# Performance work log

Hardware: AMD Instinct MI355X
Metric: run time of the kernel (lower is better)

The kernel has to match this reference:

```python
import jax, jax.numpy as jnp
import numpy as np

T = 2048          # num tokens
H_DIM = 2048      # hidden_size
NUM_HEADS = 32    # linear_num_value_heads
NUM_KV = 16       # linear_num_key_heads
DK = 128          # linear_key_head_dim
DV = 128          # linear_value_head_dim
KCONV = 4         # linear_conv_kernel_dim
KEY_DIM = NUM_KV * DK       # 2048
VAL_DIM = NUM_HEADS * DV    # 4096
CHUNK = 64


def setup_inputs() -> dict:
    key = jax.random.key(0)
    ks = jax.random.split(key, 14)
    s = 0.02
    return {
        "hidden_states": jax.random.normal(ks[0], (T, H_DIM), jnp.float32),
        "Wq": jax.random.normal(ks[1], (H_DIM, KEY_DIM), jnp.float32) * s,
        "Wk": jax.random.normal(ks[2], (H_DIM, KEY_DIM), jnp.float32) * s,
        "Wv": jax.random.normal(ks[3], (H_DIM, VAL_DIM), jnp.float32) * s,
        "Wa": jax.random.normal(ks[4], (H_DIM, NUM_HEADS), jnp.float32) * s,
        "Wb": jax.random.normal(ks[5], (H_DIM, NUM_HEADS), jnp.float32) * s,
        "Wg": jax.random.normal(ks[6], (H_DIM, VAL_DIM), jnp.float32) * s,
        "conv_q": jax.random.normal(ks[7], (KEY_DIM, KCONV), jnp.float32) * 0.3,
        "conv_k": jax.random.normal(ks[8], (KEY_DIM, KCONV), jnp.float32) * 0.3,
        "conv_v": jax.random.normal(ks[9], (VAL_DIM, KCONV), jnp.float32) * 0.3,
        "dt_bias": jax.random.normal(ks[10], (NUM_HEADS,), jnp.float32) * 0.1,
        "A_log": jnp.log(jax.random.uniform(ks[11], (NUM_HEADS,), jnp.float32, 1.0, 8.0)),
        "o_norm_weight": 1.0 + 0.1 * jax.random.normal(ks[12], (DV,), jnp.float32),
        "Wo": jax.random.normal(ks[13], (VAL_DIM, H_DIM), jnp.float32) * s,
    }


def _causal_depthwise_conv(x, w):
    # x: [T, C], w: [C, K] -> causal depthwise conv, output [T, C]
    K = w.shape[1]
    xp = jnp.pad(x, ((K - 1, 0), (0, 0)))
    out = jax.lax.conv_general_dilated(
        xp.T[None], w[:, None, :], window_strides=(1,), padding='VALID',
        dimension_numbers=('NCH', 'OIH', 'NCH'), feature_group_count=w.shape[0])
    return out[0].T


def _l2norm(x, eps=1e-6):
    return x * jax.lax.rsqrt(jnp.sum(x * x, axis=-1, keepdims=True) + eps)


def _gdn_core(q, k, v, g, beta):
    # q,k: [T,H,DK]; v: [T,H,DV]; g,beta: [T,H]. Gated delta-rule recurrence,
    # scanned in chunks (rematerialized inner scan = chunked selective scan).
    def step(S, inp):
        qt, kt, vt, gt, bt = inp
        S = S * jnp.exp(gt)[:, None, None]                  # decay state [H,DK,DV]
        kv = jnp.einsum('hk,hkv->hv', kt, S)                # read memory at k
        dv = bt[:, None] * (vt - kv)                        # delta update
        S = S + kt[:, :, None] * dv[:, None, :]             # write outer(k, dv)
        o = jnp.einsum('hk,hkv->hv', qt, S)                 # read at q
        return S, o

    def chunk_fn(S, ch):
        return jax.lax.scan(step, S, ch)

    def resh(x):
        return x.reshape(T // CHUNK, CHUNK, *x.shape[1:])

    xs = (resh(q), resh(k), resh(v), resh(g), resh(beta))
    S0 = jnp.zeros((NUM_HEADS, DK, DV), jnp.float32)
    _, o = jax.lax.scan(jax.checkpoint(chunk_fn), S0, xs)
    return o.reshape(T, NUM_HEADS, DV)


def reference(hidden_states, Wq, Wk, Wv, Wa, Wb, Wg, conv_q, conv_k, conv_v,
              dt_bias, A_log, o_norm_weight, Wo):
    h = hidden_states
    # projections
    mixed = jnp.concatenate([h @ Wq, h @ Wk, h @ Wv], axis=-1)
    # fused causal depthwise conv1d + silu over concatenated qkv
    wconv = jnp.concatenate([conv_q, conv_k, conv_v], axis=0)
    mixed = _causal_depthwise_conv(mixed, wconv)
    mixed = mixed * jax.nn.sigmoid(mixed)  # silu activation
    q, k, v = jnp.split(mixed, [KEY_DIM, 2 * KEY_DIM], axis=-1)
    q = q.reshape(T, NUM_KV, DK)
    k = k.reshape(T, NUM_KV, DK)
    v = v.reshape(T, NUM_HEADS, DV)
    ratio = NUM_HEADS // NUM_KV
    q = jnp.repeat(q, ratio, axis=1)   # GQA expand (repeat-interleave)
    k = jnp.repeat(k, ratio, axis=1)
    q = _l2norm(q)
    k = _l2norm(k)
    # fused gating: g = -exp(A_log) * softplus(a + dt_bias); beta = sigmoid(b)
    x = h @ Wa + dt_bias
    sp = jnp.where(x <= 20.0, jax.nn.softplus(x), x)  # threshold=20, beta=1
    g = -jnp.exp(A_log) * sp                          # [T, H]
    beta = jax.nn.sigmoid(h @ Wb)                     # allow_neg_eigval=False
    o = _gdn_core(q * (DK ** -0.5), k, v, g, beta)
    # gated RMSNorm (norm before gate), eps=1e-5
    gate = (h @ Wg).reshape(T, NUM_HEADS, DV)
    o = o * jax.lax.rsqrt(jnp.mean(o * o, axis=-1, keepdims=True) + 1e-5) * o_norm_weight
    o = o * (gate * jax.nn.sigmoid(gate))
    return o.reshape(T, VAL_DIM) @ Wo
```

## Files before the change

### kernel.cpp

```cpp
#include <hip/hip_runtime.h>
#include <hip/hip_bf16.h>
#include <stdint.h>
#include <stddef.h>

using bf16 = __hip_bfloat16;
typedef __attribute__((ext_vector_type(8))) short short8;
typedef __attribute__((ext_vector_type(4))) float f32x4;
typedef __attribute__((ext_vector_type(2))) float f32x2;

#define T_TOK 2048
#define HD    2048
#define NH    32
#define NKV   16
#define DKh   128
#define DVh   128

__device__ __forceinline__ void bf2f(uint32_t u, float& a, float& b) {
    union { uint32_t i; float f; } x;
    x.i = u << 16;          a = x.f;
    x.i = u & 0xffff0000u;  b = x.f;
}

__device__ __forceinline__ void gload16(const void* g, void* l) {
    __builtin_amdgcn_global_load_lds(
        (const __attribute__((address_space(1))) void*)g,
        (__attribute__((address_space(3))) void*)l, 16, 0, 0);
}

__device__ __forceinline__ void store_c(bf16* C, size_t off, float v) { C[off] = __float2bfloat16(v); }
__device__ __forceinline__ void store_c(float* C, size_t off, float v) { C[off] = v; }

template <int CTRL>
__device__ __forceinline__ float dppadd(float x) {
    int y = __builtin_amdgcn_update_dpp(0, __float_as_int(x), CTRL, 0xf, 0xf, true);
    return x + __int_as_float(y);
}
__device__ __forceinline__ void red16x2(float& x, float& y) {
    x = dppadd<0xB1>(x);  y = dppadd<0xB1>(y);
    x = dppadd<0x4E>(x);  y = dppadd<0x4E>(y);
    x = dppadd<0x141>(x); y = dppadd<0x141>(y);
    x = dppadd<0x140>(x); y = dppadd<0x140>(y);
}

__device__ __forceinline__ f32x2 pkfma(f32x2 a, f32x2 b, f32x2 c) {
    return __builtin_elementwise_fma(a, b, c);
}

__global__ __launch_bounds__(256) void f2b_kernel(
    const float* __restrict__ in, bf16* __restrict__ out, int n)
{
    int i = blockIdx.x * 256 + threadIdx.x;
    if (i < n) out[i] = __float2bfloat16(in[i]);
}

__global__ __launch_bounds__(256) void transpose_kernel(
    const float* __restrict__ in, bf16* __restrict__ out, int R, int C)
{
    __shared__ bf16 tile[32][33];
    int c0 = blockIdx.x * 32, r0 = blockIdx.y * 32;
    int x = threadIdx.x;
    int y = threadIdx.y;
    #pragma unroll
    for (int i = y; i < 32; i += 8)
        tile[i][x] = __float2bfloat16(in[(size_t)(r0 + i) * C + c0 + x]);
    __syncthreads();
    #pragma unroll
    for (int i = y; i < 32; i += 8)
        out[(size_t)(c0 + i) * R + r0 + x] = tile[x][i];
}

__global__ __launch_bounds__(256) void build_wab_kernel(
    const float* __restrict__ Wa, const float* __restrict__ Wb, bf16* __restrict__ out)
{
    int k = blockIdx.x * 256 + threadIdx.x;
    int n = blockIdx.y;
    float v = 0.f;
    if (n < 32)      v = Wa[(size_t)k * 32 + n];
    else if (n < 64) v = Wb[(size_t)k * 32 + (n - 32)];
    out[(size_t)n * 2048 + k] = __float2bfloat16(v);
}

template <typename OutT>
__global__ __launch_bounds__(256) void gemm_bt_kernel(
    const bf16* __restrict__ A, const bf16* __restrict__ B, OutT* __restrict__ C,
    int M, int N, int K)
{
    __shared__ short sA[128 * 64];
    __shared__ short sB[128 * 64];
    const int tid  = threadIdx.x;
    const int w    = tid >> 6;
    const int lane = tid & 63;
    const int quad = lane >> 4;
    const int r    = lane & 15;
    const int wm   = w >> 1, wn = w & 1;
    const int bm   = blockIdx.x, bn = blockIdx.y;
    const int lrow = lane >> 3;
    const int lp   = lane & 7;
    const int lc   = lp ^ lrow;

    f32x4 acc[4][4] = {};

    const int nkb = K >> 6;
    for (int kb = 0; kb < nkb; ++kb) {
        __syncthreads();
        #pragma unroll
        for (int it = 0; it < 4; ++it) {
            int grp = w * 4 + it;
            int rr  = grp * 8 + lrow;
            const bf16* ga = A + (size_t)(bm * 128 + rr) * K + kb * 64 + lc * 8;
            gload16(ga, (void*)(sA + grp * 512));
            const bf16* gb = B + (size_t)(bn * 128 + rr) * K + kb * 64 + lc * 8;
            gload16(gb, (void*)(sB + grp * 512));
        }
        __syncthreads();

        #pragma unroll
        for (int kk = 0; kk < 2; ++kk) {
            short8 av[4], bv[4];
            #pragma unroll
            for (int i = 0; i < 4; ++i) {
                int p   = (kk * 4 + quad) ^ (r & 7);
                int row = wm * 64 + i * 16 + r;
                av[i] = *(const short8*)(sA + row * 64 + p * 8);
                int rowb = wn * 64 + i * 16 + r;
                bv[i] = *(const short8*)(sB + rowb * 64 + p * 8);
            }
            #pragma unroll
            for (int i = 0; i < 4; ++i)
                #pragma unroll
                for (int j = 0; j < 4; ++j)
                    acc[i][j] = __builtin_amdgcn_mfma_f32_16x16x32_bf16(
                        av[i], bv[j], acc[i][j], 0, 0, 0);
        }
    }

    #pragma unroll
    for (int i = 0; i < 4; ++i) {
        int row0 = bm * 128 + wm * 64 + i * 16 + quad * 4;
        #pragma unroll
        for (int j = 0; j < 4; ++j) {
            int col = bn * 128 + wn * 64 + j * 16 + r;
            #pragma unroll
            for (int e = 0; e < 4; ++e)
                store_c(C, (size_t)(row0 + e) * N + col, acc[i][j][e]);
        }
    }
}

__global__ __launch_bounds__(128) void conv_qk_kernel(
    const bf16* __restrict__ mixed, const float* __restrict__ cq,
    const float* __restrict__ ck, float* __restrict__ qn, float* __restrict__ kn,
    float* __restrict__ pk4)
{
    int t   = blockIdx.x;
    int hkv = blockIdx.y;
    int d   = threadIdx.x;
    int cl  = hkv * DKh + d;
    float aq = 0.f, ak = 0.f;
    #pragma unroll
    for (int j = 0; j < 4; ++j) {
        int ts = t - 3 + j;
        if (ts >= 0) {
            aq += __bfloat162float(mixed[(size_t)ts * 8192 + cl])        * cq[cl * 4 + j];
            ak += __bfloat162float(mixed[(size_t)ts * 8192 + 2048 + cl]) * ck[cl * 4 + j];
        }
    }
    float sq = aq / (1.f + __expf(-aq));
    float sk = ak / (1.f + __expf(-ak));
    float s0 = sq * sq, s1 = sk * sk, s2 = sq * sk;
    #pragma unroll
    for (int m = 1; m < 64; m <<= 1) {
        s0 += __shfl_xor(s0, m, 64);
        s1 += __shfl_xor(s1, m, 64);
        s2 += __shfl_xor(s2, m, 64);
    }
    __shared__ float part[6];
    if ((threadIdx.x & 63) == 0) {
        int w = threadIdx.x >> 6;
        part[w * 3 + 0] = s0; part[w * 3 + 1] = s1; part[w * 3 + 2] = s2;
    }
    __syncthreads();
    float sumq = part[0] + part[3];
    float sumk = part[1] + part[4];
    float sqk  = part[2] + part[5];
    float rnq = rsqrtf(sumq + 1e-6f);
    float rnk = rsqrtf(sumk + 1e-6f);
    const float scale = 0.08838834764831845f;
    qn[(size_t)t * 2048 + cl] = sq * rnq * scale;
    kn[(size_t)t * 2048 + cl] = sk * rnk;
    if (d == 0) {
        float qk = sqk * rnq * rnk * scale;
        pk4[((size_t)(2 * hkv)     * T_TOK + t) * 4 + 3] = qk;
        pk4[((size_t)(2 * hkv + 1) * T_TOK + t) * 4 + 3] = qk;
    }
}

__global__ __launch_bounds__(256) void conv_v_kernel(
    const bf16* __restrict__ mixed, const float* __restrict__ cv, bf16* __restrict__ vv)
{
    int idx = blockIdx.x * 256 + threadIdx.x;
    int t = idx >> 12, c = idx & 4095;
    float acc = 0.f;
    #pragma unroll
    for (int j = 0; j < 4; ++j) {
        int ts = t - 3 + j;
        if (ts >= 0)
            acc += __bfloat162float(mixed[(size_t)ts * 8192 + 4096 + c]) * cv[c * 4 + j];
    }
    vv[idx] = __float2bfloat16(acc / (1.f + __expf(-acc)));
}

__global__ __launch_bounds__(256) void gating_kernel(
    const float* __restrict__ ab, const float* __restrict__ dt_bias,
    const float* __restrict__ A_log, float* __restrict__ pk4)
{
    int i = blockIdx.x * 256 + threadIdx.x;
    int h = i >> 11, t = i & 2047;
    float a  = ab[(size_t)t * 128 + h] + dt_bias[h];
    float sp = (a <= 20.f) ? log1pf(__expf(a)) : a;
    float gg = -__expf(A_log[h]) * sp;
    float b  = ab[(size_t)t * 128 + 32 + h];
    float eg = __expf(gg);
    float be = 1.f / (1.f + __expf(-b));
    size_t base = ((size_t)h * T_TOK + t) * 4;
    pk4[base + 0] = eg;
    pk4[base + 1] = -be * eg;
    pk4[base + 2] = be;
}

__device__ __forceinline__ void gdn_step(
    f32x2 S[4], float4 kfa, float4 kfb, float4 qfa, float4 qfb,
    float egt, float nbt, float bvt, float qkt, bf16* optr, bool writer)
{
    f32x2 k2[4] = {{kfa.x, kfa.y}, {kfa.z, kfa.w}, {kfb.x, kfb.y}, {kfb.z, kfb.w}};
    f32x2 q2[4] = {{qfa.x, qfa.y}, {qfa.z, qfa.w}, {qfb.x, qfb.y}, {qfb.z, qfb.w}};
    f32x2 pd = pkfma(S[1], k2[1], S[0] * k2[0]);
    f32x2 pe = pkfma(S[3], k2[3], S[2] * k2[2]);
    f32x2 qd = pkfma(S[1], q2[1], S[0] * q2[0]);
    f32x2 qe = pkfma(S[3], q2[3], S[2] * q2[2]);
    f32x2 e2 = {egt, egt};
    f32x2 Se0 = S[0] * e2, Se1 = S[1] * e2, Se2 = S[2] * e2, Se3 = S[3] * e2;
    f32x2 ps = pd + pe;
    f32x2 qs = qd + qe;
    float d1 = ps.x + ps.y;
    float d2 = qs.x + qs.y;
    red16x2(d1, d2);
    float dvv = fmaf(nbt, d1, bvt);
    f32x2 dv2 = {dvv, dvv};
    S[0] = pkfma(k2[0], dv2, Se0);
    S[1] = pkfma(k2[1], dv2, Se1);
    S[2] = pkfma(k2[2], dv2, Se2);
    S[3] = pkfma(k2[3], dv2, Se3);
    if (writer) *optr = __float2bfloat16(fmaf(qkt, dvv, egt * d2));
}

#define TILE 16

__global__ __launch_bounds__(256, 1) void recur_kernel(
    const float* __restrict__ qn, const float* __restrict__ kn, const bf16* __restrict__ vv,
    const float* __restrict__ pk4, bf16* __restrict__ o)
{
    __shared__ float    skq[2][TILE][256];
    __shared__ float    sgt[2][TILE][4];
    __shared__ uint16_t sv2[2][TILE][16];

    int h    = blockIdx.x;
    int sp   = blockIdx.y;
    int tid  = threadIdx.x;
    int dvl  = tid >> 4;
    int dkg  = tid & 15;
    int dv   = sp * 16 + dvl;
    int hkv  = h >> 1;
    int wave = tid >> 6;
    int lane = tid & 63;
    bool writer = (dkg == 0);

    bf16* optr = o + (size_t)h * DVh + dv;

    const float* kqsrc = (lane < 32)
        ? (kn + (size_t)hkv * DKh + (size_t)lane * 4)
        : (qn + (size_t)hkv * DKh + (size_t)(lane - 32) * 4);
    const bf16*  vsrc  = vv + (size_t)h * DVh + sp * 16 + (size_t)(lane & 1) * 8;
    const float* gsrc  = pk4 + ((size_t)h * T_TOK) * 4;

    f32x2 S[4] = {};

    auto stage = [&](int b, int t0) {
        #pragma unroll
        for (int i = 0; i < 4; ++i) {
            int tok = wave * 4 + i;
            gload16(kqsrc + (size_t)(t0 + tok) * 2048, (void*)&skq[b][tok][0]);
        }
        if (wave == 0) {
            if (lane < 32)
                gload16(vsrc + (size_t)(t0 + (lane >> 1)) * 4096, (void*)&sv2[b][0][0]);
        } else if (wave == 1) {
            if (lane < 16)
                gload16(gsrc + (size_t)(t0 + lane) * 4, (void*)&sgt[b][0][0]);
        }
    };

    stage(0, 0);
    __syncthreads();

    int buf = 0;
    #pragma unroll 1
    for (int t0 = 0; t0 < T_TOK; t0 += TILE) {
        stage(buf ^ 1, t0 + TILE);
        #pragma unroll
        for (int s = 0; s < TILE; ++s) {
            const float* tokp = &skq[buf][s][0];
            float4 kA = *(const float4*)(tokp + dkg * 4);
            float4 kB = *(const float4*)(tokp + 64 + dkg * 4);
            float4 qA = *(const float4*)(tokp + 128 + dkg * 4);
            float4 qB = *(const float4*)(tokp + 192 + dkg * 4);
            float4 g4 = *(const float4*)(&sgt[buf][s][0]);
            uint32_t vu = sv2[buf][s][dvl];
            float vf = __uint_as_float(vu << 16);
            float bvt = g4.z * vf;
            gdn_step(S, kA, kB, qA, qB, g4.x, g4.y, bvt, g4.w,
                     optr + (size_t)(t0 + s) * 4096, writer);
        }
        __syncthreads();
        buf ^= 1;
    }
}

__global__ __launch_bounds__(256) void normgate_kernel(
    const bf16* __restrict__ o, const bf16* __restrict__ gate,
    const float* __restrict__ w, bf16* __restrict__ og)
{
    int grp  = blockIdx.x * 4 + (threadIdx.x >> 6);
    int lane = threadIdx.x & 63;
    int t = grp >> 5, h = grp & 31;
    size_t base = (size_t)t * 4096 + h * DVh;
    uint32_t uo = *(const uint32_t*)(o + base + lane * 2);
    float a, b; bf2f(uo, a, b);
    float ss = a * a + b * b;
    #pragma unroll
    for (int m = 1; m < 64; m <<= 1) ss += __shfl_xor(ss, m, 64);
    float rn = rsqrtf(ss * (1.f / 128.f) + 1e-5f);
    uint32_t ug = *(const uint32_t*)(gate + base + lane * 2);
    float ga, gb; bf2f(ug, ga, gb);
    float wa = w[lane * 2], wb = w[lane * 2 + 1];
    float oa = a * rn * wa * (ga / (1.f + __expf(-ga)));
    float ob = b * rn * wb * (gb / (1.f + __expf(-gb)));
    og[base + lane * 2]     = __float2bfloat16(oa);
    og[base + lane * 2 + 1] = __float2bfloat16(ob);
}

extern "C" void kernel_launch(void* const* d_in, const int* in_sizes, int n_in,
                              void* d_out, int out_size, void* d_ws, size_t ws_size,
                              hipStream_t stream)
{
    const float* h       = (const float*)d_in[0];
    const float* Wq      = (const float*)d_in[1];
    const float* Wk      = (const float*)d_in[2];
    const float* Wv      = (const float*)d_in[3];
    const float* Wa      = (const float*)d_in[4];
    const float* Wb      = (const float*)d_in[5];
    const float* Wg      = (const float*)d_in[6];
    const float* conv_q  = (const float*)d_in[7];
    const float* conv_k  = (const float*)d_in[8];
    const float* conv_v  = (const float*)d_in[9];
    const float* dt_bias = (const float*)d_in[10];
    const float* A_log   = (const float*)d_in[11];
    const float* onw     = (const float*)d_in[12];
    const float* Wo      = (const float*)d_in[13];
    float* out = (float*)d_out;

    char* ws = (char*)d_ws;
    bf16*  WqkvT = (bf16*)ws;   ws += (size_t)8192 * 2048 * 2;
    bf16*  WgT   = (bf16*)ws;   ws += (size_t)4096 * 2048 * 2;
    bf16*  WoT   = (bf16*)ws;   ws += (size_t)2048 * 4096 * 2;
    bf16*  WabT  = (bf16*)ws;   ws += (size_t)128 * 2048 * 2;
    bf16*  hb    = (bf16*)ws;   ws += (size_t)2048 * 2048 * 2;
    bf16*  mixed = (bf16*)ws;   ws += (size_t)2048 * 8192 * 2;
    float* ab    = (float*)ws;  ws += (size_t)2048 * 128 * 4;
    float* knb   = (float*)ws;  ws += (size_t)2048 * 2048 * 4;
    bf16*  vvb   = (bf16*)ws;   ws += (size_t)2048 * 4096 * 2;
    float* pk4   = (float*)ws;  ws += (size_t)NH * T_TOK * 4 * 4;
    ws += 32768;
    float* qnb = (float*)WgT;
    bf16*  ob   = WqkvT;
    bf16*  gate = WqkvT + (size_t)2048 * 4096;
    bf16*  og   = mixed;

    dim3 tb(32, 8);
    transpose_kernel<<<dim3(64, 64),  tb, 0, stream>>>(Wq, WqkvT,                       2048, 2048);
    transpose_kernel<<<dim3(64, 64),  tb, 0, stream>>>(Wk, WqkvT + (size_t)2048 * 2048, 2048, 2048);
    transpose_kernel<<<dim3(128, 64), tb, 0, stream>>>(Wv, WqkvT + (size_t)4096 * 2048, 2048, 4096);
    transpose_kernel<<<dim3(128, 64), tb, 0, stream>>>(Wg, WgT,                         2048, 4096);
    transpose_kernel<<<dim3(64, 128), tb, 0, stream>>>(Wo, WoT,                         4096, 2048);
    build_wab_kernel<<<dim3(8, 128), 256, 0, stream>>>(Wa, Wb, WabT);
    f2b_kernel<<<16384, 256, 0, stream>>>(h, hb, 2048 * 2048);

    gemm_bt_kernel<bf16> <<<dim3(16, 64), 256, 0, stream>>>(hb, WqkvT, mixed, 2048, 8192, 2048);
    gemm_bt_kernel<float><<<dim3(16, 1),  256, 0, stream>>>(hb, WabT,  ab,    2048, 128,  2048);
    gemm_bt_kernel<bf16> <<<dim3(16, 32), 256, 0, stream>>>(hb, WgT,   gate,  2048, 4096, 2048);

    conv_qk_kernel<<<dim3(2048, 16), 128, 0, stream>>>(mixed, conv_q, conv_k, qnb, knb, pk4);
    conv_v_kernel<<<32768, 256, 0, stream>>>(mixed, conv_v, vvb);
    gating_kernel<<<256, 256, 0, stream>>>(ab, dt_bias, A_log, pk4);

    recur_kernel<<<dim3(32, 8), 256, 0, stream>>>(qnb, knb, vvb, pk4, ob);
    normgate_kernel<<<16384, 256, 0, stream>>>(ob, gate, onw, og);

    gemm_bt_kernel<float><<<dim3(16, 16), 256, 0, stream>>>(og, WoT, out, 2048, 2048, 4096);
}
```

Baseline: 951.6 us.

## Process recurrence two tokens per step using precomputed cross-token dot products

Rewrites the gated delta-rule recurrence to advance two tokens at once. Both tokens' S·k and S·q reductions are issued against the same state and combined into one DPP reduction. A new kernel precomputes k_t·k_{t-1} and q_t·k_{t-1} so the second token's terms can be corrected algebraically, and the state update for the pair is fused. This roughly halves the serial reduction-latency chain per token, at the cost of an extra kernel launch, extra staged data, and a different floating-point summation order.

```diff
diff --git a/kernel.cpp b/kernel.cpp
--- a/kernel.cpp
+++ b/kernel.cpp
@@ -35,16 +35,17 @@
     int y = __builtin_amdgcn_update_dpp(0, __float_as_int(x), CTRL, 0xf, 0xf, true);
     return x + __int_as_float(y);
 }
-__device__ __forceinline__ void red16x2(float& x, float& y) {
-    x = dppadd<0xB1>(x);  y = dppadd<0xB1>(y);
-    x = dppadd<0x4E>(x);  y = dppadd<0x4E>(y);
-    x = dppadd<0x141>(x); y = dppadd<0x141>(y);
-    x = dppadd<0x140>(x); y = dppadd<0x140>(y);
+__device__ __forceinline__ void red16x4(float& a, float& b, float& c, float& d) {
+    a = dppadd<0xB1>(a);  b = dppadd<0xB1>(b);  c = dppadd<0xB1>(c);  d = dppadd<0xB1>(d);
+    a = dppadd<0x4E>(a);  b = dppadd<0x4E>(b);  c = dppadd<0x4E>(c);  d = dppadd<0x4E>(d);
+    a = dppadd<0x141>(a); b = dppadd<0x141>(b); c = dppadd<0x141>(c); d = dppadd<0x141>(d);
+    a = dppadd<0x140>(a); b = dppadd<0x140>(b); c = dppadd<0x140>(c); d = dppadd<0x140>(d);
 }
 
 __device__ __forceinline__ f32x2 pkfma(f32x2 a, f32x2 b, f32x2 c) {
     return __builtin_elementwise_fma(a, b, c);
 }
+__device__ __forceinline__ f32x2 sp2(float x) { return f32x2{x, x}; }
 
 __global__ __launch_bounds__(256) void f2b_kernel(
     const float* __restrict__ in, bf16* __restrict__ out, int n)
@@ -195,6 +196,37 @@
     }
 }
 
+__global__ __launch_bounds__(128) void xterm_kernel(
+    const float* __restrict__ qn, const float* __restrict__ kn, float* __restrict__ pcx)
+{
+    int t   = blockIdx.x * 2 + 1;
+    int hkv = blockIdx.y;
+    int cl  = hkv * DKh + threadIdx.x;
+    float kc = kn[(size_t)t * 2048 + cl];
+    float kp = kn[(size_t)(t - 1) * 2048 + cl];
+    float qc = qn[(size_t)t * 2048 + cl];
+    float s1 = kc * kp, s2 = qc * kp;
+    #pragma unroll
+    for (int m = 1; m < 64; m <<= 1) {
+        s1 += __shfl_xor(s1, m, 64);
+        s2 += __shfl_xor(s2, m, 64);
+    }
+    __shared__ float part[4];
+    if ((threadIdx.x & 63) == 0) {
+        int w = threadIdx.x >> 6;
+        part[w * 2 + 0] = s1; part[w * 2 + 1] = s2;
+    }
+    __syncthreads();
+    if (threadIdx.x == 0) {
+        float kk = part[0] + part[2];
+        float qp = part[1] + part[3];
+        size_t b0 = ((size_t)(2 * hkv)     * T_TOK + t) * 2;
+        size_t b1 = ((size_t)(2 * hkv + 1) * T_TOK + t) * 2;
+        pcx[b0] = kk; pcx[b0 + 1] = qp;
+        pcx[b1] = kk; pcx[b1 + 1] = qp;
+    }
+}
+
 __global__ __launch_bounds__(256) void conv_v_kernel(
     const bf16* __restrict__ mixed, const float* __restrict__ cv, bf16* __restrict__ vv)
 {
@@ -228,40 +260,15 @@
     pk4[base + 2] = be;
 }
 
-__device__ __forceinline__ void gdn_step(
-    f32x2 S[4], float4 kfa, float4 kfb, float4 qfa, float4 qfb,
-    float egt, float nbt, float bvt, float qkt, bf16* optr, bool writer)
-{
-    f32x2 k2[4] = {{kfa.x, kfa.y}, {kfa.z, kfa.w}, {kfb.x, kfb.y}, {kfb.z, kfb.w}};
-    f32x2 q2[4] = {{qfa.x, qfa.y}, {qfa.z, qfa.w}, {qfb.x, qfb.y}, {qfb.z, qfb.w}};
-    f32x2 pd = pkfma(S[1], k2[1], S[0] * k2[0]);
-    f32x2 pe = pkfma(S[3], k2[3], S[2] * k2[2]);
-    f32x2 qd = pkfma(S[1], q2[1], S[0] * q2[0]);
-    f32x2 qe = pkfma(S[3], q2[3], S[2] * q2[2]);
-    f32x2 e2 = {egt, egt};
-    f32x2 Se0 = S[0] * e2, Se1 = S[1] * e2, Se2 = S[2] * e2, Se3 = S[3] * e2;
-    f32x2 ps = pd + pe;
-    f32x2 qs = qd + qe;
-    float d1 = ps.x + ps.y;
-    float d2 = qs.x + qs.y;
-    red16x2(d1, d2);
-    float dvv = fmaf(nbt, d1, bvt);
-    f32x2 dv2 = {dvv, dvv};
-    S[0] = pkfma(k2[0], dv2, Se0);
-    S[1] = pkfma(k2[1], dv2, Se1);
-    S[2] = pkfma(k2[2], dv2, Se2);
-    S[3] = pkfma(k2[3], dv2, Se3);
-    if (writer) *optr = __float2bfloat16(fmaf(qkt, dvv, egt * d2));
-}
-
 #define TILE 16
 
 __global__ __launch_bounds__(256, 1) void recur_kernel(
     const float* __restrict__ qn, const float* __restrict__ kn, const bf16* __restrict__ vv,
-    const float* __restrict__ pk4, bf16* __restrict__ o)
+    const float* __restrict__ pk4, const float* __restrict__ pcx, bf16* __restrict__ o)
 {
     __shared__ float    skq[2][TILE][256];
     __shared__ float    sgt[2][TILE][4];
+    __shared__ float    sgx[2][TILE][2];
     __shared__ uint16_t sv2[2][TILE][16];
 
     int h    = blockIdx.x;
@@ -282,6 +289,7 @@
         : (qn + (size_t)hkv * DKh + (size_t)(lane - 32) * 4);
     const bf16*  vsrc  = vv + (size_t)h * DVh + sp * 16 + (size_t)(lane & 1) * 8;
     const float* gsrc  = pk4 + ((size_t)h * T_TOK) * 4;
+    const float* xsrc  = pcx + ((size_t)h * T_TOK) * 2;
 
     f32x2 S[4] = {};
 
@@ -297,6 +305,9 @@
         } else if (wave == 1) {
             if (lane < 16)
                 gload16(gsrc + (size_t)(t0 + lane) * 4, (void*)&sgt[b][0][0]);
+        } else if (wave == 2) {
+            if (lane < 8)
+                gload16(xsrc + (size_t)(t0 + lane * 2) * 2, (void*)&sgx[b][0][0]);
         }
     };
 
@@ -308,18 +319,69 @@
     for (int t0 = 0; t0 < T_TOK; t0 += TILE) {
         stage(buf ^ 1, t0 + TILE);
         #pragma unroll
-        for (int s = 0; s < TILE; ++s) {
-            const float* tokp = &skq[buf][s][0];
-            float4 kA = *(const float4*)(tokp + dkg * 4);
-            float4 kB = *(const float4*)(tokp + 64 + dkg * 4);
-            float4 qA = *(const float4*)(tokp + 128 + dkg * 4);
-            float4 qB = *(const float4*)(tokp + 192 + dkg * 4);
-            float4 g4 = *(const float4*)(&sgt[buf][s][0]);
-            uint32_t vu = sv2[buf][s][dvl];
-            float vf = __uint_as_float(vu << 16);
-            float bvt = g4.z * vf;
-            gdn_step(S, kA, kB, qA, qB, g4.x, g4.y, bvt, g4.w,
-                     optr + (size_t)(t0 + s) * 4096, writer);
+        for (int p = 0; p < TILE / 2; ++p) {
+            int s0 = 2 * p, s1 = s0 + 1;
+            const float* tp0 = &skq[buf][s0][0];
+            const float* tp1 = &skq[buf][s1][0];
+            f32x2 k0[4], q0[4], k1[4], q1[4];
+            {
+                float4 a = *(const float4*)(tp0 + dkg * 4);
+                float4 b = *(const float4*)(tp0 + 64 + dkg * 4);
+                float4 c = *(const float4*)(tp0 + 128 + dkg * 4);
+                float4 d = *(const float4*)(tp0 + 192 + dkg * 4);
+                k0[0] = {a.x, a.y}; k0[1] = {a.z, a.w}; k0[2] = {b.x, b.y}; k0[3] = {b.z, b.w};
+                q0[0] = {c.x, c.y}; q0[1] = {c.z, c.w}; q0[2] = {d.x, d.y}; q0[3] = {d.z, d.w};
+            }
+            {
+                float4 a = *(const float4*)(tp1 + dkg * 4);
+                float4 b = *(const float4*)(tp1 + 64 + dkg * 4);
+                float4 c = *(const float4*)(tp1 + 128 + dkg * 4);
+                float4 d = *(const float4*)(tp1 + 192 + dkg * 4);
+                k1[0] = {a.x, a.y}; k1[1] = {a.z, a.w}; k1[2] = {b.x, b.y}; k1[3] = {b.z, b.w};
+                q1[0] = {c.x, c.y}; q1[1] = {c.z, c.w}; q1[2] = {d.x, d.y}; q1[3] = {d.z, d.w};
+            }
+            float4 g0 = *(const float4*)(&sgt[buf][s0][0]);
+            float4 g1 = *(const float4*)(&sgt[buf][s1][0]);
+            float2 cx = *(const float2*)(&sgx[buf][s1][0]);
+            float v0 = __uint_as_float((uint32_t)sv2[buf][s0][dvl] << 16);
+            float v1 = __uint_as_float((uint32_t)sv2[buf][s1][dvl] << 16);
+
+            f32x2 pa = pkfma(S[1], k0[1], S[0] * k0[0]);
+            f32x2 pb = pkfma(S[3], k0[3], S[2] * k0[2]);
+            f32x2 qa = pkfma(S[1], q0[1], S[0] * q0[0]);
+            f32x2 qb = pkfma(S[3], q0[3], S[2] * q0[2]);
+            f32x2 ra = pkfma(S[1], k1[1], S[0] * k1[0]);
+            f32x2 rb = pkfma(S[3], k1[3], S[2] * k1[2]);
+            f32x2 sa = pkfma(S[1], q1[1], S[0] * q1[0]);
+            f32x2 sb = pkfma(S[3], q1[3], S[2] * q1[2]);
+            f32x2 ps = pa + pb, qs = qa + qb, rs = ra + rb, ss = sa + sb;
+            float D1a = ps.x + ps.y;
+            float D2a = qs.x + qs.y;
+            float D1b = rs.x + rs.y;
+            float D2b = ss.x + ss.y;
+            red16x4(D1a, D2a, D1b, D2b);
+
+            float bv0  = g0.z * v0;
+            float bv1  = g1.z * v1;
+            float dvv0 = fmaf(g0.y, D1a, bv0);
+            float d1b  = fmaf(cx.x, dvv0, g0.x * D1b);
+            float dvv1 = fmaf(g1.y, d1b, bv1);
+
+            f32x2 eev = sp2(g0.x * g1.x);
+            f32x2 d0v = sp2(dvv0 * g1.x);
+            f32x2 d1v = sp2(dvv1);
+            S[0] = pkfma(k1[0], d1v, pkfma(k0[0], d0v, S[0] * eev));
+            S[1] = pkfma(k1[1], d1v, pkfma(k0[1], d0v, S[1] * eev));
+            S[2] = pkfma(k1[2], d1v, pkfma(k0[2], d0v, S[2] * eev));
+            S[3] = pkfma(k1[3], d1v, pkfma(k0[3], d0v, S[3] * eev));
+
+            if (writer) {
+                float o0  = fmaf(g0.w, dvv0, g0.x * D2a);
+                float d2b = fmaf(cx.y, dvv0, g0.x * D2b);
+                float o1  = fmaf(g1.w, dvv1, g1.x * d2b);
+                optr[(size_t)(t0 + s0) * 4096] = __float2bfloat16(o0);
+                optr[(size_t)(t0 + s1) * 4096] = __float2bfloat16(o1);
+            }
         }
         __syncthreads();
         buf ^= 1;
@@ -380,6 +442,7 @@
     float* knb   = (float*)ws;  ws += (size_t)2048 * 2048 * 4;
     bf16*  vvb   = (bf16*)ws;   ws += (size_t)2048 * 4096 * 2;
     float* pk4   = (float*)ws;  ws += (size_t)NH * T_TOK * 4 * 4;
+    float* pcx   = (float*)ws;  ws += (size_t)NH * T_TOK * 2 * 4;
     ws += 32768;
     float* qnb = (float*)WgT;
     bf16*  ob   = WqkvT;
@@ -402,8 +465,9 @@
     conv_qk_kernel<<<dim3(2048, 16), 128, 0, stream>>>(mixed, conv_q, conv_k, qnb, knb, pk4);
     conv_v_kernel<<<32768, 256, 0, stream>>>(mixed, conv_v, vvb);
     gating_kernel<<<256, 256, 0, stream>>>(ab, dt_bias, A_log, pk4);
-
-    recur_kernel<<<dim3(32, 8), 256, 0, stream>>>(qnb, knb, vvb, pk4, ob);
+    xterm_kernel<<<dim3(1024, 16), 128, 0, stream>>>(qnb, knb, pcx);
+
+    recur_kernel<<<dim3(32, 8), 256, 0, stream>>>(qnb, knb, vvb, pk4, pcx, ob);
     normgate_kernel<<<16384, 256, 0, stream>>>(ob, gate, onw, og);
 
     gemm_bt_kernel<float><<<dim3(16, 16), 256, 0, stream>>>(og, WoT, out, 2048, 2048, 4096);
```

New measurement: 910.2 us. 1.05x faster.

## Block the delta-rule recurrence four tokens at a time using precomputed cross terms

Applied to the files above, without the earlier changes.

Adds a kernel that precomputes pairwise k·k and q·k dot products within each group of four tokens. The recurrence then does one batched set of S·k and S·q reductions and one combined state update per group, where it used to do one per token. This shortens the serial dependency chain of cross-lane DPP reductions, which set the latency of the recurrent loop. In exchange it adds an extra kernel launch, extra global traffic, more register pressure, and a different floating-point association order.

```diff
diff --git a/kernel.cpp b/kernel.cpp
--- a/kernel.cpp
+++ b/kernel.cpp
@@ -35,16 +35,22 @@
     int y = __builtin_amdgcn_update_dpp(0, __float_as_int(x), CTRL, 0xf, 0xf, true);
     return x + __int_as_float(y);
 }
-__device__ __forceinline__ void red16x2(float& x, float& y) {
-    x = dppadd<0xB1>(x);  y = dppadd<0xB1>(y);
-    x = dppadd<0x4E>(x);  y = dppadd<0x4E>(y);
-    x = dppadd<0x141>(x); y = dppadd<0x141>(y);
-    x = dppadd<0x140>(x); y = dppadd<0x140>(y);
+__device__ __forceinline__ void red16x8(float& a, float& b, float& c, float& d,
+                                        float& e, float& f, float& g, float& h) {
+    a = dppadd<0xB1>(a);  b = dppadd<0xB1>(b);  c = dppadd<0xB1>(c);  d = dppadd<0xB1>(d);
+    e = dppadd<0xB1>(e);  f = dppadd<0xB1>(f);  g = dppadd<0xB1>(g);  h = dppadd<0xB1>(h);
+    a = dppadd<0x4E>(a);  b = dppadd<0x4E>(b);  c = dppadd<0x4E>(c);  d = dppadd<0x4E>(d);
+    e = dppadd<0x4E>(e);  f = dppadd<0x4E>(f);  g = dppadd<0x4E>(g);  h = dppadd<0x4E>(h);
+    a = dppadd<0x141>(a); b = dppadd<0x141>(b); c = dppadd<0x141>(c); d = dppadd<0x141>(d);
+    e = dppadd<0x141>(e); f = dppadd<0x141>(f); g = dppadd<0x141>(g); h = dppadd<0x141>(h);
+    a = dppadd<0x140>(a); b = dppadd<0x140>(b); c = dppadd<0x140>(c); d = dppadd<0x140>(d);
+    e = dppadd<0x140>(e); f = dppadd<0x140>(f); g = dppadd<0x140>(g); h = dppadd<0x140>(h);
 }
 
 __device__ __forceinline__ f32x2 pkfma(f32x2 a, f32x2 b, f32x2 c) {
     return __builtin_elementwise_fma(a, b, c);
 }
+__device__ __forceinline__ f32x2 sp2(float x) { return f32x2{x, x}; }
 
 __global__ __launch_bounds__(256) void f2b_kernel(
     const float* __restrict__ in, bf16* __restrict__ out, int n)
@@ -195,6 +201,41 @@
     }
 }
 
+__global__ __launch_bounds__(128) void xterm_kernel(
+    const float* __restrict__ qn, const float* __restrict__ kn, float* __restrict__ pcx)
+{
+    int g   = blockIdx.x;
+    int hkv = blockIdx.y;
+    int d   = threadIdx.x;
+    int cl  = hkv * DKh + d;
+    int t0  = g * 4;
+    float k0 = kn[(size_t)(t0 + 0) * 2048 + cl];
+    float k1 = kn[(size_t)(t0 + 1) * 2048 + cl];
+    float k2 = kn[(size_t)(t0 + 2) * 2048 + cl];
+    float k3 = kn[(size_t)(t0 + 3) * 2048 + cl];
+    float q1 = qn[(size_t)(t0 + 1) * 2048 + cl];
+    float q2 = qn[(size_t)(t0 + 2) * 2048 + cl];
+    float q3 = qn[(size_t)(t0 + 3) * 2048 + cl];
+    float s[12] = {k1 * k0, k2 * k0, k2 * k1, k3 * k0, k3 * k1, k3 * k2,
+                   q1 * k0, q2 * k0, q2 * k1, q3 * k0, q3 * k1, q3 * k2};
+    #pragma unroll
+    for (int m = 1; m < 64; m <<= 1)
+        #pragma unroll
+        for (int i = 0; i < 12; ++i) s[i] += __shfl_xor(s[i], m, 64);
+    __shared__ float part[2][12];
+    if ((d & 63) == 0) {
+        int w = d >> 6;
+        #pragma unroll
+        for (int i = 0; i < 12; ++i) part[w][i] = s[i];
+    }
+    __syncthreads();
+    if (d < 12) {
+        float v = part[0][d] + part[1][d];
+        pcx[((size_t)(2 * hkv)     * 512 + g) * 12 + d] = v;
+        pcx[((size_t)(2 * hkv + 1) * 512 + g) * 12 + d] = v;
+    }
+}
+
 __global__ __launch_bounds__(256) void conv_v_kernel(
     const bf16* __restrict__ mixed, const float* __restrict__ cv, bf16* __restrict__ vv)
 {
@@ -228,40 +269,15 @@
     pk4[base + 2] = be;
 }
 
-__device__ __forceinline__ void gdn_step(
-    f32x2 S[4], float4 kfa, float4 kfb, float4 qfa, float4 qfb,
-    float egt, float nbt, float bvt, float qkt, bf16* optr, bool writer)
-{
-    f32x2 k2[4] = {{kfa.x, kfa.y}, {kfa.z, kfa.w}, {kfb.x, kfb.y}, {kfb.z, kfb.w}};
-    f32x2 q2[4] = {{qfa.x, qfa.y}, {qfa.z, qfa.w}, {qfb.x, qfb.y}, {qfb.z, qfb.w}};
-    f32x2 pd = pkfma(S[1], k2[1], S[0] * k2[0]);
-    f32x2 pe = pkfma(S[3], k2[3], S[2] * k2[2]);
-    f32x2 qd = pkfma(S[1], q2[1], S[0] * q2[0]);
-    f32x2 qe = pkfma(S[3], q2[3], S[2] * q2[2]);
-    f32x2 e2 = {egt, egt};
-    f32x2 Se0 = S[0] * e2, Se1 = S[1] * e2, Se2 = S[2] * e2, Se3 = S[3] * e2;
-    f32x2 ps = pd + pe;
-    f32x2 qs = qd + qe;
-    float d1 = ps.x + ps.y;
-    float d2 = qs.x + qs.y;
-    red16x2(d1, d2);
-    float dvv = fmaf(nbt, d1, bvt);
-    f32x2 dv2 = {dvv, dvv};
-    S[0] = pkfma(k2[0], dv2, Se0);
-    S[1] = pkfma(k2[1], dv2, Se1);
-    S[2] = pkfma(k2[2], dv2, Se2);
-    S[3] = pkfma(k2[3], dv2, Se3);
-    if (writer) *optr = __float2bfloat16(fmaf(qkt, dvv, egt * d2));
-}
-
 #define TILE 16
 
 __global__ __launch_bounds__(256, 1) void recur_kernel(
     const float* __restrict__ qn, const float* __restrict__ kn, const bf16* __restrict__ vv,
-    const float* __restrict__ pk4, bf16* __restrict__ o)
+    const float* __restrict__ pk4, const float* __restrict__ pcx, bf16* __restrict__ o)
 {
     __shared__ float    skq[2][TILE][256];
     __shared__ float    sgt[2][TILE][4];
+    __shared__ float    sgx[2][48];
     __shared__ uint16_t sv2[2][TILE][16];
 
     int h    = blockIdx.x;
@@ -282,6 +298,7 @@
         : (qn + (size_t)hkv * DKh + (size_t)(lane - 32) * 4);
     const bf16*  vsrc  = vv + (size_t)h * DVh + sp * 16 + (size_t)(lane & 1) * 8;
     const float* gsrc  = pk4 + ((size_t)h * T_TOK) * 4;
+    const float* xsrc  = pcx + (size_t)h * 512 * 12;
 
     f32x2 S[4] = {};
 
@@ -297,6 +314,9 @@
         } else if (wave == 1) {
             if (lane < 16)
                 gload16(gsrc + (size_t)(t0 + lane) * 4, (void*)&sgt[b][0][0]);
+        } else if (wave == 2) {
+            if (lane < 12)
+                gload16(xsrc + (size_t)(t0 >> 2) * 12 + (size_t)lane * 4, (void*)&sgx[b][0]);
         }
     };
 
@@ -308,18 +328,87 @@
     for (int t0 = 0; t0 < T_TOK; t0 += TILE) {
         stage(buf ^ 1, t0 + TILE);
         #pragma unroll
-        for (int s = 0; s < TILE; ++s) {
-            const float* tokp = &skq[buf][s][0];
-            float4 kA = *(const float4*)(tokp + dkg * 4);
-            float4 kB = *(const float4*)(tokp + 64 + dkg * 4);
-            float4 qA = *(const float4*)(tokp + 128 + dkg * 4);
-            float4 qB = *(const float4*)(tokp + 192 + dkg * 4);
-            float4 g4 = *(const float4*)(&sgt[buf][s][0]);
-            uint32_t vu = sv2[buf][s][dvl];
-            float vf = __uint_as_float(vu << 16);
-            float bvt = g4.z * vf;
-            gdn_step(S, kA, kB, qA, qB, g4.x, g4.y, bvt, g4.w,
-                     optr + (size_t)(t0 + s) * 4096, writer);
+        for (int gi = 0; gi < 4; ++gi) {
+            int s0 = gi * 4;
+            f32x2 kv[4][4], qv[4][4];
+            #pragma unroll
+            for (int tt = 0; tt < 4; ++tt) {
+                const float* tp = &skq[buf][s0 + tt][0];
+                float4 a = *(const float4*)(tp + dkg * 4);
+                float4 b = *(const float4*)(tp + 64 + dkg * 4);
+                float4 c = *(const float4*)(tp + 128 + dkg * 4);
+                float4 d = *(const float4*)(tp + 192 + dkg * 4);
+                kv[tt][0] = {a.x, a.y}; kv[tt][1] = {a.z, a.w};
+                kv[tt][2] = {b.x, b.y}; kv[tt][3] = {b.z, b.w};
+                qv[tt][0] = {c.x, c.y}; qv[tt][1] = {c.z, c.w};
+                qv[tt][2] = {d.x, d.y}; qv[tt][3] = {d.z, d.w};
+            }
+            float4 g0 = *(const float4*)(&sgt[buf][s0 + 0][0]);
+            float4 g1 = *(const float4*)(&sgt[buf][s0 + 1][0]);
+            float4 g2 = *(const float4*)(&sgt[buf][s0 + 2][0]);
+            float4 g3 = *(const float4*)(&sgt[buf][s0 + 3][0]);
+            const float* cxp = &sgx[buf][gi * 12];
+            float4 cxA = *(const float4*)(cxp);
+            float4 cxB = *(const float4*)(cxp + 4);
+            float4 cxC = *(const float4*)(cxp + 8);
+            float v0 = __uint_as_float((uint32_t)sv2[buf][s0 + 0][dvl] << 16);
+            float v1 = __uint_as_float((uint32_t)sv2[buf][s0 + 1][dvl] << 16);
+            float v2 = __uint_as_float((uint32_t)sv2[buf][s0 + 2][dvl] << 16);
+            float v3 = __uint_as_float((uint32_t)sv2[buf][s0 + 3][dvl] << 16);
+
+            f32x2 pK0 = pkfma(S[3], kv[0][3], S[2] * kv[0][2]) + pkfma(S[1], kv[0][1], S[0] * kv[0][0]);
+            f32x2 pQ0 = pkfma(S[3], qv[0][3], S[2] * qv[0][2]) + pkfma(S[1], qv[0][1], S[0] * qv[0][0]);
+            f32x2 pK1 = pkfma(S[3], kv[1][3], S[2] * kv[1][2]) + pkfma(S[1], kv[1][1], S[0] * kv[1][0]);
+            f32x2 pQ1 = pkfma(S[3], qv[1][3], S[2] * qv[1][2]) + pkfma(S[1], qv[1][1], S[0] * qv[1][0]);
+            f32x2 pK2 = pkfma(S[3], kv[2][3], S[2] * kv[2][2]) + pkfma(S[1], kv[2][1], S[0] * kv[2][0]);
+            f32x2 pQ2 = pkfma(S[3], qv[2][3], S[2] * qv[2][2]) + pkfma(S[1], qv[2][1], S[0] * qv[2][0]);
+            f32x2 pK3 = pkfma(S[3], kv[3][3], S[2] * kv[3][2]) + pkfma(S[1], kv[3][1], S[0] * kv[3][0]);
+            f32x2 pQ3 = pkfma(S[3], qv[3][3], S[2] * qv[3][2]) + pkfma(S[1], qv[3][1], S[0] * qv[3][0]);
+            float K0 = pK0.x + pK0.y, Q0 = pQ0.x + pQ0.y;
+            float K1 = pK1.x + pK1.y, Q1 = pQ1.x + pQ1.y;
+            float K2 = pK2.x + pK2.y, Q2 = pQ2.x + pQ2.y;
+            float K3 = pK3.x + pK3.y, Q3 = pQ3.x + pQ3.y;
+            red16x8(K0, Q0, K1, Q1, K2, Q2, K3, Q3);
+
+            float e0 = g0.x, e1 = g1.x, e2 = g2.x, e3 = g3.x;
+            float e01 = e0 * e1, e12 = e1 * e2, e012 = e01 * e2;
+            float bv0 = g0.z * v0, bv1 = g1.z * v1, bv2 = g2.z * v2, bv3 = g3.z * v3;
+            float dvv0 = fmaf(g0.y, K0, bv0);
+            float d1   = fmaf(cxA.x, dvv0, e0 * K1);
+            float dvv1 = fmaf(g1.y, d1, bv1);
+            float d2p  = fmaf(e1 * cxA.y, dvv0, e01 * K2);
+            float d2   = fmaf(cxA.z, dvv1, d2p);
+            float dvv2 = fmaf(g2.y, d2, bv2);
+            float d3p  = fmaf(e12 * cxA.w, dvv0, e012 * K3);
+            d3p        = fmaf(e2 * cxB.x, dvv1, d3p);
+            float d3   = fmaf(cxB.y, dvv2, d3p);
+            float dvv3 = fmaf(g3.y, d3, bv3);
+
+            float e23 = e2 * e3, e123 = e1 * e23, eall = e0 * e123;
+            f32x2 ev = sp2(eall);
+            f32x2 c0 = sp2(e123 * dvv0), c1 = sp2(e23 * dvv1);
+            f32x2 c2 = sp2(e3 * dvv2),   c3 = sp2(dvv3);
+            #pragma unroll
+            for (int j = 0; j < 4; ++j)
+                S[j] = pkfma(kv[3][j], c3, pkfma(kv[2][j], c2,
+                       pkfma(kv[1][j], c1, pkfma(kv[0][j], c0, S[j] * ev))));
+
+            if (writer) {
+                float o0  = fmaf(g0.w, dvv0, e0 * Q0);
+                float q1p = fmaf(cxB.z, dvv0, e0 * Q1);
+                float o1  = fmaf(g1.w, dvv1, e1 * q1p);
+                float q2p = fmaf(e1 * cxB.w, dvv0, e01 * Q2);
+                q2p       = fmaf(cxC.x, dvv1, q2p);
+                float o2  = fmaf(g2.w, dvv2, e2 * q2p);
+                float q3p = fmaf(e12 * cxC.y, dvv0, e012 * Q3);
+                q3p       = fmaf(e2 * cxC.z, dvv1, q3p);
+                q3p       = fmaf(cxC.w, dvv2, q3p);
+                float o3  = fmaf(g3.w, dvv3, e3 * q3p);
+                optr[(size_t)(t0 + s0 + 0) * 4096] = __float2bfloat16(o0);
+                optr[(size_t)(t0 + s0 + 1) * 4096] = __float2bfloat16(o1);
+                optr[(size_t)(t0 + s0 + 2) * 4096] = __float2bfloat16(o2);
+                optr[(size_t)(t0 + s0 + 3) * 4096] = __float2bfloat16(o3);
+            }
         }
         __syncthreads();
         buf ^= 1;
@@ -380,6 +469,7 @@
     float* knb   = (float*)ws;  ws += (size_t)2048 * 2048 * 4;
     bf16*  vvb   = (bf16*)ws;   ws += (size_t)2048 * 4096 * 2;
     float* pk4   = (float*)ws;  ws += (size_t)NH * T_TOK * 4 * 4;
+    float* pcx   = (float*)ws;  ws += (size_t)NH * 512 * 12 * 4;
     ws += 32768;
     float* qnb = (float*)WgT;
     bf16*  ob   = WqkvT;
@@ -402,8 +492,9 @@
     conv_qk_kernel<<<dim3(2048, 16), 128, 0, stream>>>(mixed, conv_q, conv_k, qnb, knb, pk4);
     conv_v_kernel<<<32768, 256, 0, stream>>>(mixed, conv_v, vvb);
     gating_kernel<<<256, 256, 0, stream>>>(ab, dt_bias, A_log, pk4);
-
-    recur_kernel<<<dim3(32, 8), 256, 0, stream>>>(qnb, knb, vvb, pk4, ob);
+    xterm_kernel<<<dim3(512, 16), 128, 0, stream>>>(qnb, knb, pcx);
+
+    recur_kernel<<<dim3(32, 8), 256, 0, stream>>>(qnb, knb, vvb, pk4, pcx, ob);
     normgate_kernel<<<16384, 256, 0, stream>>>(ob, gate, onw, og);
 
     gemm_bt_kernel<float><<<dim3(16, 16), 256, 0, stream>>>(og, WoT, out, 2048, 2048, 4096);
```

Result: faster. 895.2 us (-5.9%).
